# Performance work log

Hardware: AMD Instinct MI355X
Metric: run time of the kernel (lower is better)

## Reference

```python
import jax, jax.numpy as jnp
import numpy as np
from jax import lax

T, B, IN_DIM, HID, OUT = 101, 16384, 40, 300, 12
TAU, VTH, SG_ALPHA = 2.0, 1.0, 2.0


@jax.custom_vjp
def spike(x):
    # Heaviside spike with ATan surrogate gradient (spikingjelly-style).
    return (x >= 0.0).astype(x.dtype)

def _spike_fwd(x):
    return spike(x), x

def _spike_bwd(x, g):
    sg = (SG_ALPHA / 2.0) / (1.0 + (jnp.pi / 2.0 * SG_ALPHA * x) ** 2)
    return (g * sg,)

spike.defvjp(_spike_fwd, _spike_bwd)


def _lif(v, cur):
    # LIFNode, decay_input=True, hard reset to 0:
    # v <- v + (cur - v)/tau ; s = H(v - vth) ; v <- v*(1-s)
    v = v + (cur - v) / TAU
    s = spike(v - VTH)
    return v * (1.0 - s), s


def setup_inputs() -> dict:
    key = jax.random.key(0)
    ks = jax.random.split(key, 9)
    def lin(k, fan_in, shape):
        bound = 1.0 / np.sqrt(fan_in)
        return jax.random.uniform(k, shape, jnp.float32, -bound, bound)
    return {
        "x": jax.random.normal(ks[0], (T, B, IN_DIM), jnp.float32),
        "W1": lin(ks[1], IN_DIM, (HID, IN_DIM)),
        "b1": lin(ks[2], IN_DIM, (HID,)),
        "Wh": lin(ks[3], HID, (HID, HID)),
        "bh": lin(ks[4], HID, (HID,)),
        "W2": lin(ks[5], HID, (HID, HID)),
        "b2": lin(ks[6], HID, (HID,)),
        "W3": lin(ks[7], HID, (OUT, HID)),
        "b3": lin(ks[8], HID, (OUT,)),
    }


def reference(x, W1, b1, Wh, bh, W2, b2, W3, b3):
    # Dropout layers are identity in eval mode.
    # Input linear (40->300) is time-independent: batch it across T up front.
    h1 = jnp.einsum('tbi,hi->tbh', x, W1) + b1          # [T,B,300]
    zB = jnp.zeros((x.shape[1], HID), x.dtype)

    def step(carry, h1_t):
        y, v1, v2 = carry
        # RecurrentContainer: y = LIF( hid_weight(y) + x_t )
        cur1 = y @ Wh.T + bh + h1_t                      # [B,300]
        v1, y = _lif(v1, cur1)
        # feedforward Linear(300,300) + LIF
        v2, s2 = _lif(v2, y @ W2.T + b2)
        out_t = s2 @ W3.T + b3                           # [B,12]
        return (y, v1, v2), out_t

    _, outs = lax.scan(step, (zB, zB, zB), h1)           # outs: [T,B,12]
    return outs.sum(0)                                   # res.sum(0)
```

## Files before the change

### kernel.cpp

```cpp
#include <hip/hip_runtime.h>

#define T_STEPS 101
#define BATCH   16384
#define IN_DIM  40
#define HID     300
#define OUT_DIM 12

#define RPW 4
#define WPB 8
#define RPB (RPW * WPB)
#define NTHREADS (WPB * 64)

#define WS_W2T 96000
#define WS_W3T 192000

template<int I> struct ic { static constexpr int v = I; };
template<int N, int I = 0, typename F>
__device__ __forceinline__ void sfor(F&& f) {
    if constexpr (I < N) {
        f(ic<I>{});
        sfor<N, I + 1, F>(static_cast<F&&>(f));
    }
}

__global__ __launch_bounds__(256) void prep_kernel(const float* __restrict__ Wh,
                                                   const float* __restrict__ W2,
                                                   const float* __restrict__ W3,
                                                   float* __restrict__ ws) {
    int idx = blockIdx.x * 256 + threadIdx.x;
    if (idx < 96000) {
        int i = idx / 320, j = idx % 320;
        ws[idx] = (j < HID) ? Wh[j * HID + i] : 0.f;
    } else if (idx < 192000) {
        int k = idx - 96000;
        int i = k / 320, j = k % 320;
        ws[idx] = (j < HID) ? W2[j * HID + i] : 0.f;
    } else if (idx < 195600) {
        int k = idx - 192000;
        int i = k / OUT_DIM, j = k % OUT_DIM;
        ws[idx] = W3[j * HID + i];
    }
}

__device__ __forceinline__ void walk4(const float* __restrict__ base,
                                      unsigned long long m0, unsigned long long m1,
                                      unsigned long long m2, unsigned long long m3,
                                      float (&a0)[5], float (&a1)[5],
                                      float (&a2)[5], float (&a3)[5]) {
    while (m0 | m1 | m2 | m3) {
        const bool h0 = (m0 != 0ull), h1 = (m1 != 0ull), h2 = (m2 != 0ull), h3 = (m3 != 0ull);
        const int b0 = h0 ? (int)__builtin_ctzll(m0) : 0;
        const int b1 = h1 ? (int)__builtin_ctzll(m1) : 0;
        const int b2 = h2 ? (int)__builtin_ctzll(m2) : 0;
        const int b3 = h3 ? (int)__builtin_ctzll(m3) : 0;
        m0 &= m0 - 1; m1 &= m1 - 1; m2 &= m2 - 1; m3 &= m3 - 1;
        const float g0 = h0 ? 1.0f : 0.0f;
        const float g1 = h1 ? 1.0f : 0.0f;
        const float g2 = h2 ? 1.0f : 0.0f;
        const float g3 = h3 ? 1.0f : 0.0f;
        const float* p0 = base + b0 * 320;
        const float* p1 = base + b1 * 320;
        const float* p2 = base + b2 * 320;
        const float* p3 = base + b3 * 320;
        float l0[5], l1[5], l2[5], l3[5];
        sfor<5>([&](auto uc) { constexpr int u = decltype(uc)::v; l0[u] = p0[64 * u]; });
        sfor<5>([&](auto uc) { constexpr int u = decltype(uc)::v; l1[u] = p1[64 * u]; });
        sfor<5>([&](auto uc) { constexpr int u = decltype(uc)::v; l2[u] = p2[64 * u]; });
        sfor<5>([&](auto uc) { constexpr int u = decltype(uc)::v; l3[u] = p3[64 * u]; });
        sfor<5>([&](auto uc) { constexpr int u = decltype(uc)::v; a0[u] = fmaf(g0, l0[u], a0[u]); });
        sfor<5>([&](auto uc) { constexpr int u = decltype(uc)::v; a1[u] = fmaf(g1, l1[u], a1[u]); });
        sfor<5>([&](auto uc) { constexpr int u = decltype(uc)::v; a2[u] = fmaf(g2, l2[u], a2[u]); });
        sfor<5>([&](auto uc) { constexpr int u = decltype(uc)::v; a3[u] = fmaf(g3, l3[u], a3[u]); });
    }
}

__global__ __launch_bounds__(NTHREADS, 2) void snn_kernel(
    const float* __restrict__ x,
    const float* __restrict__ W1,
    const float* __restrict__ b1,
    const float* __restrict__ bh,
    const float* __restrict__ b2,
    const float* __restrict__ b3,
    const float* __restrict__ ws,
    float* __restrict__ out)
{
    __shared__ float w1c[10 * 320 * 4];
    __shared__ float oacc[RPB][OUT_DIM];

    const int tid  = threadIdx.x;
    const int lane = tid & 63;
    const int wv   = __builtin_amdgcn_readfirstlane(tid >> 6);
    const int row0 = blockIdx.x * RPB;

    for (int idx = tid; idx < 3200; idx += NTHREADS) {
        int kc = idx % 10;
        int j  = idx / 10;
        float4 v;
        if (j < HID) v = *(const float4*)(W1 + j * IN_DIM + kc * 4);
        else         v = make_float4(0.f, 0.f, 0.f, 0.f);
        *(float4*)(w1c + (kc * 320 + j) * 4) = v;
    }
    for (int idx = tid; idx < RPB * OUT_DIM; idx += NTHREADS) ((float*)oacc)[idx] = 0.f;

    float b1h[5], b2r[5];
    sfor<5>([&](auto uc) {
        constexpr int u = decltype(uc)::v;
        int j = lane + 64 * u;
        b1h[u] = (j < HID) ? (b1[j] + bh[j]) : 0.f;
        b2r[u] = (j < HID) ? b2[j] : 0.f;
    });

    const float* WhT = ws;
    const float* W2T = ws + WS_W2T;
    const float* W3T = ws + WS_W3T;

    float v1[RPW][5], v2[RPW][5];
    unsigned long long pm[RPW][5];
    sfor<RPW>([&](auto rc) {
        constexpr int r = decltype(rc)::v;
        sfor<5>([&](auto uc) {
            constexpr int u = decltype(uc)::v;
            v1[r][u] = 0.f; v2[r][u] = 0.f; pm[r][u] = 0ull;
        });
    });

    __syncthreads();

    const unsigned long long TAILMASK = (1ull << 44) - 1ull;

    for (int t = 0; t < T_STEPS; ++t) {
        const float* xt = x + ((size_t)t * BATCH + row0 + wv * RPW) * IN_DIM;

        float acc[RPW][5];
        sfor<RPW>([&](auto rc) {
            constexpr int r = decltype(rc)::v;
            sfor<5>([&](auto uc) {
                constexpr int u = decltype(uc)::v;
                acc[r][u] = b1h[u];
            });
        });

        sfor<10>([&](auto kcc) {
            constexpr int kc = decltype(kcc)::v;
            float4 w[5];
            sfor<5>([&](auto uc) {
                constexpr int u = decltype(uc)::v;
                w[u] = *(const float4*)(w1c + (kc * 320 + lane + 64 * u) * 4);
            });
            sfor<RPW>([&](auto rc) {
                constexpr int r = decltype(rc)::v;
                const float* xr = xt + r * IN_DIM + kc * 4;
                float x0 = xr[0], x1 = xr[1], x2 = xr[2], x3 = xr[3];
                sfor<5>([&](auto uc) {
                    constexpr int u = decltype(uc)::v;
                    float a = acc[r][u];
                    a = fmaf(w[u].x, x0, a);
                    a = fmaf(w[u].y, x1, a);
                    a = fmaf(w[u].z, x2, a);
                    a = fmaf(w[u].w, x3, a);
                    acc[r][u] = a;
                });
            });
        });

        sfor<5>([&](auto u2c) {
            constexpr int u2 = decltype(u2c)::v;
            walk4(WhT + u2 * 64 * 320 + lane,
                  pm[0][u2], pm[1][u2], pm[2][u2], pm[3][u2],
                  acc[0], acc[1], acc[2], acc[3]);
        });

        sfor<RPW>([&](auto rc) {
            constexpr int r = decltype(rc)::v;
            sfor<5>([&](auto uc) {
                constexpr int u = decltype(uc)::v;
                float v = v1[r][u];
                v = v + (acc[r][u] - v) * 0.5f;
                bool s = (v >= 1.0f);
                v1[r][u] = s ? 0.f : v;
                pm[r][u] = __ballot(s);
            });
            pm[r][4] &= TAILMASK;
        });

        float c2[RPW][5];
        sfor<RPW>([&](auto rc) {
            constexpr int r = decltype(rc)::v;
            sfor<5>([&](auto uc) {
                constexpr int u = decltype(uc)::v;
                c2[r][u] = b2r[u];
            });
        });
        sfor<5>([&](auto u2c) {
            constexpr int u2 = decltype(u2c)::v;
            walk4(W2T + u2 * 64 * 320 + lane,
                  pm[0][u2], pm[1][u2], pm[2][u2], pm[3][u2],
                  c2[0], c2[1], c2[2], c2[3]);
        });

        sfor<RPW>([&](auto rc) {
            constexpr int r = decltype(rc)::v;
            unsigned long long sm[5];
            sfor<5>([&](auto uc) {
                constexpr int u = decltype(uc)::v;
                float v = v2[r][u];
                v = v + (c2[r][u] - v) * 0.5f;
                bool s = (v >= 1.0f);
                v2[r][u] = s ? 0.f : v;
                sm[u] = __ballot(s);
            });
            sm[4] &= TAILMASK;
            const int lr = wv * RPW + r;
            sfor<5>([&](auto u2c) {
                constexpr int u2 = decltype(u2c)::v;
                unsigned long long m = sm[u2];
                while (m) {
                    int b = __builtin_ctzll(m);
                    m &= m - 1;
                    if (lane < OUT_DIM)
                        oacc[lr][lane] += W3T[(u2 * 64 + b) * OUT_DIM + lane];
                }
            });
        });
    }

    __syncthreads();

    for (int idx = tid; idx < RPB * OUT_DIM; idx += NTHREADS) {
        int r = idx / OUT_DIM, o = idx % OUT_DIM;
        out[(size_t)(row0 + r) * OUT_DIM + o] = oacc[r][o] + 101.0f * b3[o];
    }
}

extern "C" void kernel_launch(void* const* d_in, const int* in_sizes, int n_in,
                              void* d_out, int out_size, void* d_ws, size_t ws_size,
                              hipStream_t stream) {
    const float* x  = (const float*)d_in[0];
    const float* W1 = (const float*)d_in[1];
    const float* b1 = (const float*)d_in[2];
    const float* Wh = (const float*)d_in[3];
    const float* bh = (const float*)d_in[4];
    const float* W2 = (const float*)d_in[5];
    const float* b2 = (const float*)d_in[6];
    const float* W3 = (const float*)d_in[7];
    const float* b3 = (const float*)d_in[8];
    float* out = (float*)d_out;
    float* ws  = (float*)d_ws;

    prep_kernel<<<(195600 + 255) / 256, 256, 0, stream>>>(Wh, W2, W3, ws);
    snn_kernel<<<BATCH / RPB, NTHREADS, 0, stream>>>(x, W1, b1, bh, b2, b3, ws, out);
}
```

Baseline: 2.806 ms.

## Prefetch next-step input rows into double-buffered LDS with nontemporal loads

Before, every lane issued scalar global loads of the same x values for its wave's rows inside the W1 loop. Now 40 lanes of each wave issue one vector nontemporal load each for step t+1 at the top of step t, and write it into a per-wave double-buffered LDS slot at the end of the step. The W1 loop reads x from LDS and is reordered to load one W1 float4 at a time, which cuts live registers. The aim is to hide global-load latency behind the recurrent work and remove redundant broadcast loads, at the cost of a small LDS buffer and one register-held prefetch.

```diff
diff --git a/kernel.cpp b/kernel.cpp
--- a/kernel.cpp
+++ b/kernel.cpp
@@ -10,6 +10,8 @@
 #define WPB 8
 #define RPB (RPW * WPB)
 #define NTHREADS (WPB * 64)
+
+typedef float f4 __attribute__((ext_vector_type(4)));
 
 #define WS_W2T 96000
 #define WS_W3T 192000
@@ -86,6 +88,7 @@
 {
     __shared__ float w1c[10 * 320 * 4];
     __shared__ float oacc[RPB][OUT_DIM];
+    __shared__ f4 xs[WPB][2][RPW][10];
 
     const int tid  = threadIdx.x;
     const int lane = tid & 63;
@@ -102,6 +105,16 @@
     }
     for (int idx = tid; idx < RPB * OUT_DIM; idx += NTHREADS) ((float*)oacc)[idx] = 0.f;
 
+    const int lr_r = lane / 10;
+    const int lkc  = lane - lr_r * 10;
+    const float* xbase = x + (size_t)(row0 + wv * RPW + lr_r) * IN_DIM + lkc * 4;
+
+    {
+        f4 nx0 = {0.f, 0.f, 0.f, 0.f};
+        if (lane < 40) nx0 = __builtin_nontemporal_load((const f4*)xbase);
+        if (lane < 40) xs[wv][0][lr_r][lkc] = nx0;
+    }
+
     float b1h[5], b2r[5];
     sfor<5>([&](auto uc) {
         constexpr int u = decltype(uc)::v;
@@ -129,7 +142,15 @@
     const unsigned long long TAILMASK = (1ull << 44) - 1ull;
 
     for (int t = 0; t < T_STEPS; ++t) {
-        const float* xt = x + ((size_t)t * BATCH + row0 + wv * RPW) * IN_DIM;
+        const int cb = t & 1;
+
+        f4 nx = {0.f, 0.f, 0.f, 0.f};
+        {
+            const int tn = (t + 1 < T_STEPS) ? t + 1 : t;
+            if (lane < 40)
+                nx = __builtin_nontemporal_load(
+                        (const f4*)(xbase + (size_t)tn * (BATCH * IN_DIM)));
+        }
 
         float acc[RPW][5];
         sfor<RPW>([&](auto rc) {
@@ -142,22 +163,21 @@
 
         sfor<10>([&](auto kcc) {
             constexpr int kc = decltype(kcc)::v;
-            float4 w[5];
-            sfor<5>([&](auto uc) {
-                constexpr int u = decltype(uc)::v;
-                w[u] = *(const float4*)(w1c + (kc * 320 + lane + 64 * u) * 4);
-            });
+            f4 xq[RPW];
             sfor<RPW>([&](auto rc) {
                 constexpr int r = decltype(rc)::v;
-                const float* xr = xt + r * IN_DIM + kc * 4;
-                float x0 = xr[0], x1 = xr[1], x2 = xr[2], x3 = xr[3];
-                sfor<5>([&](auto uc) {
-                    constexpr int u = decltype(uc)::v;
+                xq[r] = xs[wv][cb][r][kc];
+            });
+            sfor<5>([&](auto uc) {
+                constexpr int u = decltype(uc)::v;
+                float4 w = *(const float4*)(w1c + (kc * 320 + lane + 64 * u) * 4);
+                sfor<RPW>([&](auto rc) {
+                    constexpr int r = decltype(rc)::v;
                     float a = acc[r][u];
-                    a = fmaf(w[u].x, x0, a);
-                    a = fmaf(w[u].y, x1, a);
-                    a = fmaf(w[u].z, x2, a);
-                    a = fmaf(w[u].w, x3, a);
+                    a = fmaf(w.x, xq[r][0], a);
+                    a = fmaf(w.y, xq[r][1], a);
+                    a = fmaf(w.z, xq[r][2], a);
+                    a = fmaf(w.w, xq[r][3], a);
                     acc[r][u] = a;
                 });
             });
@@ -222,6 +242,8 @@
                 }
             });
         });
+
+        if (lane < 40) xs[wv][(t + 1) & 1][lr_r][lkc] = nx;
     }
 
     __syncthreads();
```

Measured after the change: 3.067 ms. 9.3% more time.
